# Performance work log

Hardware: AMD Instinct MI355X
Metric: run time of the kernel (lower is better)

The kernel has to match this reference:

```python
import jax, jax.numpy as jnp
import numpy as np

D_MODEL = 1024
N_HEADS = 16
D_FF = 4096
B, T = 4, 2048
EPS = 1e-5


def layernorm(x, g, b):
    mu = jnp.mean(x, axis=-1, keepdims=True)
    var = jnp.var(x, axis=-1, keepdims=True)
    return (x - mu) * jax.lax.rsqrt(var + EPS) * g + b


def setup_inputs() -> dict:
    key = jax.random.key(0)
    ks = jax.random.split(key, 8)
    s = 0.02
    return {
        "x": jax.random.normal(ks[0], (B, T, D_MODEL), jnp.float32),
        "ln1_g": jnp.ones((D_MODEL,), jnp.float32),
        "ln1_b": jnp.zeros((D_MODEL,), jnp.float32),
        "wq": jax.random.normal(ks[1], (D_MODEL, D_MODEL), jnp.float32) * s,
        "bq": jnp.zeros((D_MODEL,), jnp.float32),
        "wk": jax.random.normal(ks[2], (D_MODEL, D_MODEL), jnp.float32) * s,
        "bk": jnp.zeros((D_MODEL,), jnp.float32),
        "wv": jax.random.normal(ks[3], (D_MODEL, D_MODEL), jnp.float32) * s,
        "bv": jnp.zeros((D_MODEL,), jnp.float32),
        "wo": jax.random.normal(ks[4], (D_MODEL, D_MODEL), jnp.float32) * s,
        "bo": jnp.zeros((D_MODEL,), jnp.float32),
        "ln2_g": jnp.ones((D_MODEL,), jnp.float32),
        "ln2_b": jnp.zeros((D_MODEL,), jnp.float32),
        "w1": jax.random.normal(ks[5], (D_FF, D_MODEL), jnp.float32) * s,
        "b1": jnp.zeros((D_FF,), jnp.float32),
        "w2": jax.random.normal(ks[6], (D_MODEL, D_FF), jnp.float32) * s,
        "b2": jnp.zeros((D_MODEL,), jnp.float32),
    }


def reference(x, ln1_g, ln1_b, wq, bq, wk, bk, wv, bv, wo, bo,
              ln2_g, ln2_b, w1, b1, w2, b2):
    d_k = D_MODEL // N_HEADS
    # --- attention sublayer (pre-LN) ---
    h = layernorm(x, ln1_g, ln1_b)                       # [B,T,D]
    q = (h @ wq.T + bq).reshape(B, T, N_HEADS, d_k)
    k = (h @ wk.T + bk).reshape(B, T, N_HEADS, d_k)
    v = (h @ wv.T + bv).reshape(B, T, N_HEADS, d_k)
    scores = jnp.einsum("bqhd,bkhd->bhqk", q, k) / jnp.sqrt(jnp.float32(d_k))
    attn = jax.nn.softmax(scores, axis=-1)               # [B,H,T,T]
    o = jnp.einsum("bhqk,bkhd->bqhd", attn, v).reshape(B, T, D_MODEL)
    x = x + (o @ wo.T + bo)
    # --- FFN sublayer ---
    h2 = layernorm(x, ln2_g, ln2_b)
    h2 = jax.nn.gelu(h2 @ w1.T + b1, approximate=False)  # torch GELU = exact erf
    x = x + (h2 @ w2.T + b2)
    return x
```

## Files before the change

kernel.cpp:

```cpp
#include <hip/hip_runtime.h>
#include <math.h>


#define D_MODEL 1024
#define D_FF    4096
#define NH      16
#define BATCH   4
#define SEQ     2048
#define DK      64
#define MTOK    (BATCH*SEQ)
#define NBH     (BATCH*NH)

typedef __bf16 bf16;
typedef _Float16 f16;
typedef bf16  bf16x4 __attribute__((ext_vector_type(4)));
typedef bf16  bf16x8 __attribute__((ext_vector_type(8)));
typedef f16   f16x4  __attribute__((ext_vector_type(4)));
typedef f16   f16x8  __attribute__((ext_vector_type(8)));
typedef __fp16 hf16x2 __attribute__((ext_vector_type(2)));
typedef __fp16 hf16x4 __attribute__((ext_vector_type(4)));
typedef __fp16 hf16x8 __attribute__((ext_vector_type(8)));
typedef float f32x4  __attribute__((ext_vector_type(4)));

__device__ __forceinline__ void gload_lds16(const void* g, void* l) {
  __builtin_amdgcn_global_load_lds(
      (__attribute__((address_space(1))) void*)g,
      (__attribute__((address_space(3))) void*)l, 16, 0, 0);
}

#define BAR() __builtin_amdgcn_s_barrier()
#define LGKM0() do { asm volatile("s_waitcnt lgkmcnt(0)" ::: "memory"); \
  __builtin_amdgcn_sched_barrier(0); } while (0)
#define WAIT_VM0() do { asm volatile("s_waitcnt vmcnt(0)" ::: "memory"); \
  __builtin_amdgcn_sched_barrier(0); } while (0)
#define WAIT_VM4() do { asm volatile("s_waitcnt vmcnt(4)" ::: "memory"); \
  __builtin_amdgcn_sched_barrier(0); } while (0)

__device__ __forceinline__ float gelu_fast(float x) {
  float ax = fabsf(x) * 0.70710678118654752f;
  float t  = 1.0f / (1.0f + 0.3275911f * ax);
  float p  = t * (0.254829592f + t * (-0.284496736f + t * (1.421413741f +
             t * (-1.453152027f + t * 1.061405429f))));
  float e  = __builtin_amdgcn_exp2f(ax * ax * -1.4426950408889634f);
  float er = 1.0f - p * e;
  er = __builtin_copysignf(er, x);
  return 0.5f * x * (1.0f + er);
}

__global__ __launch_bounds__(256) void cast_w(const float* __restrict__ s,
                                              bf16* __restrict__ d, int n) {
  int i = (blockIdx.x * 256 + threadIdx.x) * 4;
  if (i >= n) return;
  float4 v = *(const float4*)(s + i);
  bf16x4 o;
  o[0] = (bf16)v.x; o[1] = (bf16)v.y; o[2] = (bf16)v.z; o[3] = (bf16)v.w;
  *(bf16x4*)(d + i) = o;
}

__global__ __launch_bounds__(256) void ln_kernel(const float* __restrict__ x,
                                                 const float* __restrict__ g,
                                                 const float* __restrict__ b,
                                                 bf16* __restrict__ out) {
  int row = blockIdx.x;
  int tid = threadIdx.x;
  const float* xr = x + (size_t)row * D_MODEL;
  float4 v = *(const float4*)(xr + tid * 4);
  float s  = v.x + v.y + v.z + v.w;
  float sq = v.x*v.x + v.y*v.y + v.z*v.z + v.w*v.w;
  #pragma unroll
  for (int off = 1; off < 64; off <<= 1) {
    s  += __shfl_xor(s,  off, 64);
    sq += __shfl_xor(sq, off, 64);
  }
  __shared__ float ls[4], lq[4];
  int wid = tid >> 6, lane = tid & 63;
  if (lane == 0) { ls[wid] = s; lq[wid] = sq; }
  __syncthreads();
  s  = ls[0] + ls[1] + ls[2] + ls[3];
  sq = lq[0] + lq[1] + lq[2] + lq[3];
  float mu   = s * (1.0f / D_MODEL);
  float var  = sq * (1.0f / D_MODEL) - mu * mu;
  float rstd = rsqrtf(var + 1e-5f);
  float4 gv = *(const float4*)(g + tid * 4);
  float4 bv = *(const float4*)(b + tid * 4);
  bf16x4 o;
  o[0] = (bf16)((v.x - mu) * rstd * gv.x + bv.x);
  o[1] = (bf16)((v.y - mu) * rstd * gv.y + bv.y);
  o[2] = (bf16)((v.z - mu) * rstd * gv.z + bv.z);
  o[3] = (bf16)((v.w - mu) * rstd * gv.w + bv.w);
  *(bf16x4*)(out + (size_t)row * D_MODEL + tid * 4) = o;
}

enum { EP_QKV = 0, EP_RESID = 1, EP_GELU = 2 };
#define QSCALE 0.18033688011112042f

template <int EP>
__global__ __launch_bounds__(512, 2) void gemm256(
    const bf16* __restrict__ A, const bf16* __restrict__ W,
    const float* __restrict__ bias,
    bf16* __restrict__ out_bf,
    int M, int N, int K) {
  __shared__ char lds[131072];
  int tiles_n = N >> 8;
  int nwg = (M >> 8) * tiles_n;
  int bid = blockIdx.x;
  int swz = (bid & 7) * (nwg >> 3) + (bid >> 3);
  int bm = swz / tiles_n, bn = swz % tiles_n;
  int m0 = bm << 8, n0 = bn << 8;
  int tid = threadIdx.x, wid = tid >> 6, lane = tid & 63;
  int wm = wid >> 2, wn = wid & 3;
  int l15 = lane & 15, l4 = lane >> 4;

  f32x4 acc[8][4];
  #pragma unroll
  for (int f = 0; f < 8; f++)
    #pragma unroll
    for (int n = 0; n < 4; n++)
      #pragma unroll
      for (int e = 0; e < 4; e++) acc[f][n][e] = 0.f;

  auto STAGEH = [&](int h, int kt, int bsel) {
    char* buf = lds + bsel * 65536;
    #pragma unroll
    for (int l = 0; l < 2; ++l) {
      int o = h * 16384 + l * 8192 + tid * 16;
      int row = (o >> 7) & 255;
      int g = (o >> 4) & 7;
      int gs = g ^ (row & 7);
      const bf16* src = (h < 2 ? A + (size_t)(m0 + row) * K
                               : W + (size_t)(n0 + row) * K) + kt * 64 + gs * 8;
      gload_lds16(src, buf + o);
    }
  };
  auto RDB = [&](const char* bc, int n, int kk) -> bf16x8 {
    int row = wn * 64 + n * 16 + l15;
    return *(const bf16x8*)(bc + 32768 + row * 128 + (((kk << 2) + l4) ^ (row & 7)) * 16);
  };

  int nt = K >> 6;
  STAGEH(0, 0, 0); STAGEH(1, 0, 0); STAGEH(2, 0, 0); STAGEH(3, 0, 0);
  STAGEH(0, 1, 1); STAGEH(1, 1, 1);
  WAIT_VM4();
  BAR();

  for (int t = 0; t < nt; ++t) {
    const char* bc = lds + (t & 1) * 65536;
    bf16x8 af[8][2];

    #pragma unroll
    for (int f = 0; f < 8; ++f)
      #pragma unroll
      for (int kk = 0; kk < 2; ++kk) {
        int row = wm * 128 + f * 16 + l15;
        af[f][kk] = *(const bf16x8*)(bc + row * 128 + (((kk << 2) + l4) ^ (row & 7)) * 16);
      }
    bf16x8 b0[2];
    b0[0] = RDB(bc, 0, 0); b0[1] = RDB(bc, 0, 1);
    if (t + 1 < nt) STAGEH(2, t + 1, (t + 1) & 1);
    BAR(); LGKM0();
    __builtin_amdgcn_s_setprio(1);
    #pragma unroll
    for (int f = 0; f < 8; ++f)
      #pragma unroll
      for (int kk = 0; kk < 2; ++kk) {
        if (EP == EP_QKV)
          acc[f][0] = __builtin_amdgcn_mfma_f32_16x16x32_bf16(af[f][kk], b0[kk], acc[f][0], 0, 0, 0);
        else
          acc[f][0] = __builtin_amdgcn_mfma_f32_16x16x32_bf16(b0[kk], af[f][kk], acc[f][0], 0, 0, 0);
      }
    __builtin_amdgcn_s_setprio(0);
    BAR();

    bf16x8 b1[2];
    b1[0] = RDB(bc, 1, 0); b1[1] = RDB(bc, 1, 1);
    if (t + 1 < nt) STAGEH(3, t + 1, (t + 1) & 1);
    BAR(); LGKM0();
    __builtin_amdgcn_s_setprio(1);
    #pragma unroll
    for (int f = 0; f < 8; ++f)
      #pragma unroll
      for (int kk = 0; kk < 2; ++kk) {
        if (EP == EP_QKV)
          acc[f][1] = __builtin_amdgcn_mfma_f32_16x16x32_bf16(af[f][kk], b1[kk], acc[f][1], 0, 0, 0);
        else
          acc[f][1] = __builtin_amdgcn_mfma_f32_16x16x32_bf16(b1[kk], af[f][kk], acc[f][1], 0, 0, 0);
      }
    __builtin_amdgcn_s_setprio(0);
    BAR();

    bf16x8 b2[2];
    b2[0] = RDB(bc, 2, 0); b2[1] = RDB(bc, 2, 1);
    if (t + 2 < nt) STAGEH(0, t + 2, t & 1);
    BAR(); LGKM0();
    __builtin_amdgcn_s_setprio(1);
    #pragma unroll
    for (int f = 0; f < 8; ++f)
      #pragma unroll
      for (int kk = 0; kk < 2; ++kk) {
        if (EP == EP_QKV)
          acc[f][2] = __builtin_amdgcn_mfma_f32_16x16x32_bf16(af[f][kk], b2[kk], acc[f][2], 0, 0, 0);
        else
          acc[f][2] = __builtin_amdgcn_mfma_f32_16x16x32_bf16(b2[kk], af[f][kk], acc[f][2], 0, 0, 0);
      }
    __builtin_amdgcn_s_setprio(0);
    BAR();

    bf16x8 b3[2];
    b3[0] = RDB(bc, 3, 0); b3[1] = RDB(bc, 3, 1);
    if (t + 2 < nt) STAGEH(1, t + 2, t & 1);
    BAR(); LGKM0();
    __builtin_amdgcn_s_setprio(1);
    #pragma unroll
    for (int f = 0; f < 8; ++f)
      #pragma unroll
      for (int kk = 0; kk < 2; ++kk) {
        if (EP == EP_QKV)
          acc[f][3] = __builtin_amdgcn_mfma_f32_16x16x32_bf16(af[f][kk], b3[kk], acc[f][3], 0, 0, 0);
        else
          acc[f][3] = __builtin_amdgcn_mfma_f32_16x16x32_bf16(b3[kk], af[f][kk], acc[f][3], 0, 0, 0);
      }
    __builtin_amdgcn_s_setprio(0);
    if (t + 2 < nt)      { WAIT_VM4(); }
    else if (t + 1 < nt) { WAIT_VM0(); }
    BAR();
  }

  if (EP == EP_QKV) {
    #pragma unroll
    for (int i = 0; i < 8; i++)
      #pragma unroll
      for (int j = 0; j < 4; j++) {
        int gm0 = m0 + wm * 128 + i * 16 + (l4 << 2);
        int gn  = n0 + wn * 64 + j * 16 + l15;
        int which = gn >> 10;
        int nn = gn & 1023, head = nn >> 6, d = nn & 63;
        int bb = gm0 >> 11, t = gm0 & 2047;
        float bv = bias[gn];
        if (which == 2) {
          int sbase = (t & ~31) + ((t >> 2) & 3) * 8 + ((t >> 4) & 1) * 4;
          f16x4 pk;
          #pragma unroll
          for (int jj = 0; jj < 4; jj++) pk[jj] = (f16)(acc[i][j][jj] + bv);
          *(f16x4*)((f16*)out_bf + (size_t)2 * NBH * SEQ * DK +
                    ((size_t)(bb * NH + head) * DK + d) * SEQ + sbase) = pk;
        } else {
          float scale = (which == 0) ? QSCALE : 1.0f;
          #pragma unroll
          for (int jj = 0; jj < 4; jj++) {
            float cv = (acc[i][j][jj] + bv) * scale;
            size_t idx = (size_t)which * (NBH * SEQ * DK) +
                         ((size_t)(bb * NH + head) * SEQ + (t + jj)) * DK + d;
            out_bf[idx] = (bf16)cv;
          }
        }
      }
  } else {
    #pragma unroll
    for (int i = 0; i < 8; i++) {
      int gm = m0 + wm * 128 + i * 16 + l15;
      #pragma unroll
      for (int j = 0; j < 4; j++) {
        int gn = n0 + wn * 64 + j * 16 + (l4 << 2);
        float4 bv4 = *(const float4*)(bias + gn);
        bf16x4 pk;
        pk[0] = (bf16)gelu_fast(acc[i][j][0] + bv4.x);
        pk[1] = (bf16)gelu_fast(acc[i][j][1] + bv4.y);
        pk[2] = (bf16)gelu_fast(acc[i][j][2] + bv4.z);
        pk[3] = (bf16)gelu_fast(acc[i][j][3] + bv4.w);
        *(bf16x4*)(out_bf + (size_t)gm * N + gn) = pk;
      }
    }
  }
}

__global__ __launch_bounds__(512) void gemm_resid(
    const bf16* __restrict__ A, const bf16* __restrict__ W,
    const float* __restrict__ bias,
    const float* __restrict__ resid,
    float* __restrict__ out_f32,
    int M, int N, int K) {
  constexpr int BK = 64, RB = 128;
  constexpr int AB = 16384, TB = 49152, L = 6;
  __shared__ char lds[3 * TB];

  int tiles_n = N >> 8;
  int nwg = (M >> 7) * tiles_n;
  int bid = blockIdx.x;
  int swz = (bid & 7) * (nwg >> 3) + (bid >> 3);
  int bm = swz / tiles_n, bn = swz % tiles_n;
  int m0 = bm << 7, n0 = bn << 8;
  int tid = threadIdx.x, wid = tid >> 6, lane = tid & 63;
  int wm = wid >> 2, wn = wid & 3;
  int l15 = lane & 15, l4 = lane >> 4;

  f32x4 acc[4][4];
  #pragma unroll
  for (int i = 0; i < 4; i++)
    #pragma unroll
    for (int j = 0; j < 4; j++)
      #pragma unroll
      for (int e = 0; e < 4; e++) acc[i][j][e] = 0.f;

  auto STAGE = [&](int kt, int nb) {
    char* buf = lds + nb * TB;
    #pragma unroll
    for (int l = 0; l < L; ++l) {
      bool isA = l < 2;
      int o = (isA ? l : l - 2) * 8192 + tid * 16;
      int row = o >> 7;
      int g = (o >> 4) & 7;
      int gs = g ^ (row & 7);
      const bf16* src = (isA ? A + (size_t)(m0 + row) * K
                             : W + (size_t)(n0 + row) * K) + kt * BK + gs * 8;
      gload_lds16(src, buf + (isA ? 0 : AB) + o);
    }
  };

  int nt = K / BK;
  STAGE(0, 0);
  STAGE(1, 1);
  asm volatile("s_waitcnt vmcnt(6)" ::: "memory");
  __builtin_amdgcn_sched_barrier(0);
  BAR();

  for (int t = 0; t < nt; ++t) {
    int cb = t % 3, nb = cb >= 1 ? cb - 1 : 2;
    const char* bc = lds + cb * TB;
    if (t + 2 < nt) STAGE(t + 2, nb);

    bf16x8 af[4][2], bfr[4][2];
    #pragma unroll
    for (int f = 0; f < 4; ++f)
      #pragma unroll
      for (int kk = 0; kk < 2; ++kk) {
        int row = wm * 64 + f * 16 + l15;
        af[f][kk] = *(const bf16x8*)(bc + row * RB + (((kk << 2) + l4) ^ (row & 7)) * 16);
      }
    #pragma unroll
    for (int fc = 0; fc < 4; ++fc)
      #pragma unroll
      for (int kk = 0; kk < 2; ++kk) {
        int row = wn * 64 + fc * 16 + l15;
        bfr[fc][kk] = *(const bf16x8*)(bc + AB + row * RB + (((kk << 2) + l4) ^ (row & 7)) * 16);
      }

    __builtin_amdgcn_s_setprio(1);
    #pragma unroll
    for (int f = 0; f < 4; ++f)
      #pragma unroll
      for (int fc = 0; fc < 4; ++fc)
        #pragma unroll
        for (int kk = 0; kk < 2; ++kk)
          acc[f][fc] = __builtin_amdgcn_mfma_f32_16x16x32_bf16(bfr[fc][kk], af[f][kk],
                                                               acc[f][fc], 0, 0, 0);
    __builtin_amdgcn_s_setprio(0);

    if (t + 2 < nt) {
      asm volatile("s_waitcnt vmcnt(6)" ::: "memory");
      __builtin_amdgcn_sched_barrier(0);
    } else if (t + 1 < nt) {
      WAIT_VM0();
    }
    BAR();
  }

  #pragma unroll
  for (int i = 0; i < 4; i++) {
    int gm = m0 + wm * 64 + i * 16 + l15;
    #pragma unroll
    for (int j = 0; j < 4; j++) {
      int gn = n0 + wn * 64 + j * 16 + (l4 << 2);
      float4 bv4 = *(const float4*)(bias + gn);
      size_t idx = (size_t)gm * N + gn;
      float4 rv = *(const float4*)(resid + idx);
      float4 ov;
      ov.x = rv.x + acc[i][j][0] + bv4.x;
      ov.y = rv.y + acc[i][j][1] + bv4.y;
      ov.z = rv.z + acc[i][j][2] + bv4.z;
      ov.w = rv.w + acc[i][j][3] + bv4.w;
      *(float4*)(out_f32 + idx) = ov;
    }
  }
}

__global__ __launch_bounds__(512) void attn_kernel(
    const bf16* __restrict__ q, const bf16* __restrict__ k,
    const f16* __restrict__ vt, bf16* __restrict__ o) {
  __shared__ bf16 kt_lds[2][64 * 64];
  __shared__ f16  vt_lds[2][64 * 64];
  int bid = blockIdx.x;
  int swzb = (bid & 7) * 64 + (bid >> 3);
  int bh = swzb >> 3;
  int qt = swzb & 7;
  int t0 = qt << 8;
  int tid = threadIdx.x, wid = tid >> 6, lane = tid & 63;
  int l15 = lane & 15, l4 = lane >> 4;

  int kb0 = l15 * 128 + ((l4 ^ (l15 & 7)) << 4);
  int kb1 = l15 * 128 + (((4 + l4) ^ (l15 & 7)) << 4);
  int vb32[2];
  #pragma unroll
  for (int n = 0; n < 2; n++)
    vb32[n] = l15 * 128 + (((n * 4 + l4) ^ (l15 & 7)) << 4);

  bf16x8 qf[2][2];
  #pragma unroll
  for (int qr = 0; qr < 2; qr++) {
    const bf16* qbase = q + ((size_t)bh * SEQ + t0 + wid * 32 + qr * 16 + l15) * DK;
    qf[qr][0] = *(const bf16x8*)(qbase + (l4 << 3));
    qf[qr][1] = *(const bf16x8*)(qbase + 32 + (l4 << 3));
  }

  f16x8 vones8;
  #pragma unroll
  for (int e = 0; e < 8; e++) vones8[e] = (f16)1.f;
  float m_run[2] = {-1e30f, -1e30f};
  f32x4 acc_o[2][4];
  f32x4 acc_l[2];
  #pragma unroll
  for (int qr = 0; qr < 2; qr++) {
    #pragma unroll
    for (int nd = 0; nd < 4; nd++)
      #pragma unroll
      for (int e = 0; e < 4; e++) acc_o[qr][nd][e] = 0.f;
    #pragma unroll
    for (int e = 0; e < 4; e++) acc_l[qr][e] = 0.f;
  }

  int oK = tid * 16;
  int rowk = oK >> 7, gk = (oK >> 4) & 7;
  const bf16* gKsrc = k + ((size_t)bh * SEQ + rowk) * DK + ((gk ^ (rowk & 7)) << 3);
  int dV = oK >> 7, gd = (oK >> 4) & 7;
  const f16* gVsrc = vt + ((size_t)bh * DK + dV) * SEQ + ((gd ^ (dV & 7)) << 3);

  auto stage = [&](int buf, int t) {
    int kv0 = t * 64;
    gload_lds16(gKsrc + (size_t)kv0 * DK, (char*)&kt_lds[buf][0] + tid * 16);
    gload_lds16(gVsrc + kv0, (char*)&vt_lds[buf][0] + tid * 16);
  };

  stage(0, 0);
  WAIT_VM0();
  BAR();

  for (int t = 0; t < SEQ / 64; ++t) {
    int cur = t & 1;
    if (t < SEQ / 64 - 1) stage(cur ^ 1, t + 1);
    const char* kbase = (const char*)&kt_lds[cur][0];
    const char* vbase = (const char*)&vt_lds[cur][0];

    f32x4 accs[2][4];
    #pragma unroll
    for (int qr = 0; qr < 2; qr++)
      #pragma unroll
      for (int n = 0; n < 4; n++)
        #pragma unroll
        for (int e = 0; e < 4; e++) accs[qr][n][e] = 0.f;
    __builtin_amdgcn_s_setprio(1);
    #pragma unroll
    for (int n = 0; n < 4; n++) {
      bf16x8 kf0 = *(const bf16x8*)(kbase + kb0 + n * 2048);
      bf16x8 kf1 = *(const bf16x8*)(kbase + kb1 + n * 2048);
      #pragma unroll
      for (int qr = 0; qr < 2; qr++) {
        accs[qr][n] = __builtin_amdgcn_mfma_f32_16x16x32_bf16(kf0, qf[qr][0], accs[qr][n], 0, 0, 0);
        accs[qr][n] = __builtin_amdgcn_mfma_f32_16x16x32_bf16(kf1, qf[qr][1], accs[qr][n], 0, 0, 0);
      }
    }
    __builtin_amdgcn_s_setprio(0);

    f16x8 pa32[2][2];
    #pragma unroll
    for (int qr = 0; qr < 2; qr++) {
      float mloc = -1e30f;
      #pragma unroll
      for (int n = 0; n < 4; n++) {
        float a0 = fmaxf(accs[qr][n][0], accs[qr][n][1]);
        float a1 = fmaxf(accs[qr][n][2], accs[qr][n][3]);
        mloc = fmaxf(mloc, fmaxf(a0, a1));
      }
      float mt = fmaxf(mloc, __shfl_xor(mloc, 16, 64));
      mt = fmaxf(mt, __shfl_xor(mt, 32, 64));
      if (__any(mt > m_run[qr] + 8.0f)) {
        float mn = fmaxf(m_run[qr], mt);
        float sc = __builtin_amdgcn_exp2f(m_run[qr] - mn);
        m_run[qr] = mn;
        float scr0 = __shfl(sc, l4 * 20 + 0, 64);
        float scr1 = __shfl(sc, l4 * 20 + 1, 64);
        float scr2 = __shfl(sc, l4 * 20 + 2, 64);
        float scr3 = __shfl(sc, l4 * 20 + 3, 64);
        #pragma unroll
        for (int nd = 0; nd < 4; nd++) {
          acc_o[qr][nd][0] *= scr0; acc_o[qr][nd][1] *= scr1;
          acc_o[qr][nd][2] *= scr2; acc_o[qr][nd][3] *= scr3;
        }
        acc_l[qr][0] *= scr0; acc_l[qr][1] *= scr1;
        acc_l[qr][2] *= scr2; acc_l[qr][3] *= scr3;
      }
      #pragma unroll
      for (int n = 0; n < 2; n++) {
        float e0 = __builtin_amdgcn_exp2f(accs[qr][2*n][0] - m_run[qr]);
        float e1 = __builtin_amdgcn_exp2f(accs[qr][2*n][1] - m_run[qr]);
        float e2 = __builtin_amdgcn_exp2f(accs[qr][2*n][2] - m_run[qr]);
        float e3 = __builtin_amdgcn_exp2f(accs[qr][2*n][3] - m_run[qr]);
        float e4 = __builtin_amdgcn_exp2f(accs[qr][2*n+1][0] - m_run[qr]);
        float e5 = __builtin_amdgcn_exp2f(accs[qr][2*n+1][1] - m_run[qr]);
        float e6 = __builtin_amdgcn_exp2f(accs[qr][2*n+1][2] - m_run[qr]);
        float e7 = __builtin_amdgcn_exp2f(accs[qr][2*n+1][3] - m_run[qr]);
        hf16x2 p01 = __builtin_amdgcn_cvt_pkrtz(e0, e1);
        hf16x2 p23 = __builtin_amdgcn_cvt_pkrtz(e2, e3);
        hf16x2 p45 = __builtin_amdgcn_cvt_pkrtz(e4, e5);
        hf16x2 p67 = __builtin_amdgcn_cvt_pkrtz(e6, e7);
        hf16x4 lo = __builtin_shufflevector(p01, p23, 0, 1, 2, 3);
        hf16x4 hi = __builtin_shufflevector(p45, p67, 0, 1, 2, 3);
        hf16x8 cmb = __builtin_shufflevector(lo, hi, 0, 1, 2, 3, 4, 5, 6, 7);
        pa32[qr][n] = __builtin_bit_cast(f16x8, cmb);
      }
    }

    __builtin_amdgcn_s_setprio(1);
    #pragma unroll
    for (int n = 0; n < 2; n++) {
      #pragma unroll
      for (int nd = 0; nd < 4; nd++) {
        f16x8 vf = *(const f16x8*)(vbase + vb32[n] + nd * 2048);
        #pragma unroll
        for (int qr = 0; qr < 2; qr++)
          acc_o[qr][nd] = __builtin_amdgcn_mfma_f32_16x16x32_f16(pa32[qr][n], vf, acc_o[qr][nd], 0, 0, 0);
      }
      #pragma unroll
      for (int qr = 0; qr < 2; qr++)
        acc_l[qr] = __builtin_amdgcn_mfma_f32_16x16x32_f16(pa32[qr][n], vones8, acc_l[qr], 0, 0, 0);
    }
    __builtin_amdgcn_s_setprio(0);

    if (t < SEQ / 64 - 1) { WAIT_VM0(); }
    BAR();
  }

  int bb = bh >> 4, hh = bh & 15;
  #pragma unroll
  for (int qr = 0; qr < 2; qr++) {
    float rl0 = 1.0f / acc_l[qr][0], rl1 = 1.0f / acc_l[qr][1];
    float rl2 = 1.0f / acc_l[qr][2], rl3 = 1.0f / acc_l[qr][3];
    int rowb = t0 + wid * 32 + qr * 16 + l4 * 4;
    #pragma unroll
    for (int nd = 0; nd < 4; nd++) {
      int d = nd * 16 + l15;
      o[((size_t)bb * SEQ + rowb + 0) * D_MODEL + hh * DK + d] = (bf16)(acc_o[qr][nd][0] * rl0);
      o[((size_t)bb * SEQ + rowb + 1) * D_MODEL + hh * DK + d] = (bf16)(acc_o[qr][nd][1] * rl1);
      o[((size_t)bb * SEQ + rowb + 2) * D_MODEL + hh * DK + d] = (bf16)(acc_o[qr][nd][2] * rl2);
      o[((size_t)bb * SEQ + rowb + 3) * D_MODEL + hh * DK + d] = (bf16)(acc_o[qr][nd][3] * rl3);
    }
  }
}

extern "C" void kernel_launch(void* const* d_in, const int* in_sizes, int n_in,
                              void* d_out, int out_size, void* d_ws, size_t ws_size,
                              hipStream_t stream) {
  const float* x    = (const float*)d_in[0];
  const float* ln1g = (const float*)d_in[1];
  const float* ln1b = (const float*)d_in[2];
  const float* wq   = (const float*)d_in[3];
  const float* bq   = (const float*)d_in[4];
  const float* wk   = (const float*)d_in[5];
  const float* bk   = (const float*)d_in[6];
  const float* wv   = (const float*)d_in[7];
  const float* bv   = (const float*)d_in[8];
  const float* wo   = (const float*)d_in[9];
  const float* bo   = (const float*)d_in[10];
  const float* ln2g = (const float*)d_in[11];
  const float* ln2b = (const float*)d_in[12];
  const float* w1   = (const float*)d_in[13];
  const float* b1   = (const float*)d_in[14];
  const float* w2   = (const float*)d_in[15];
  const float* b2   = (const float*)d_in[16];
  float* out = (float*)d_out;

  char* ws = (char*)d_ws;
  bf16* wqkv_b = (bf16*)(ws);
  bf16* wo_b   = (bf16*)(ws + ((size_t)6  << 20));
  bf16* w1_b   = (bf16*)(ws + ((size_t)8  << 20));
  bf16* w2_b   = (bf16*)(ws + ((size_t)16 << 20));
  bf16* h_b    = (bf16*)(ws + ((size_t)24 << 20));
  bf16* qkv_b  = (bf16*)(ws + ((size_t)40 << 20));
  bf16* o_b    = (bf16*)(ws + ((size_t)88 << 20));
  bf16* ffn1_b = (bf16*)(ws + ((size_t)40 << 20));
  float* bqkv  = (float*)(ws + ((size_t)104 << 20));

  cast_w<<<1024, 256, 0, stream>>>(wq, wqkv_b, 1 << 20);
  cast_w<<<1024, 256, 0, stream>>>(wk, wqkv_b + (1 << 20), 1 << 20);
  cast_w<<<1024, 256, 0, stream>>>(wv, wqkv_b + (2 << 20), 1 << 20);
  cast_w<<<1024, 256, 0, stream>>>(wo, wo_b, 1 << 20);
  cast_w<<<4096, 256, 0, stream>>>(w1, w1_b, 1 << 22);
  cast_w<<<4096, 256, 0, stream>>>(w2, w2_b, 1 << 22);
  (void)hipMemcpyAsync(bqkv,        bq, 4096, hipMemcpyDeviceToDevice, stream);
  (void)hipMemcpyAsync(bqkv + 1024, bk, 4096, hipMemcpyDeviceToDevice, stream);
  (void)hipMemcpyAsync(bqkv + 2048, bv, 4096, hipMemcpyDeviceToDevice, stream);

  ln_kernel<<<MTOK, 256, 0, stream>>>(x, ln1g, ln1b, h_b);
  gemm256<EP_QKV><<<384, 512, 0, stream>>>(h_b, wqkv_b, bqkv, qkv_b,
                                           MTOK, 3072, 1024);
  attn_kernel<<<512, 512, 0, stream>>>(qkv_b, qkv_b + (size_t)NBH * SEQ * DK,
                                       (const f16*)(qkv_b + (size_t)2 * NBH * SEQ * DK),
                                       o_b);
  gemm_resid<<<256, 512, 0, stream>>>(o_b, wo_b, bo, x, out, MTOK, 1024, 1024);
  ln_kernel<<<MTOK, 256, 0, stream>>>(out, ln2g, ln2b, h_b);
  gemm256<EP_GELU><<<512, 512, 0, stream>>>(h_b, w1_b, b1, ffn1_b,
                                            MTOK, 4096, 1024);
  gemm_resid<<<256, 512, 0, stream>>>(ffn1_b, w2_b, b2, out, out, MTOK, 1024, 4096);
}
```

Baseline: 392.8 us.

## Fuse weight casts and bias copies into one launch; reorder GEMM fragment loads

Replaces six weight-cast kernel launches and three device-to-device bias memcpys with a single fused kernel, cutting launch and copy overhead. Separately, the gemm256 main loop now loads the A fragments in two halves of four, interleaved with pairs of B fragments across the four phases. This lowers peak register use, at the cost of rereading some B fragments from LDS.

```diff
diff --git a/kernel.cpp b/kernel.cpp
--- a/kernel.cpp
+++ b/kernel.cpp
@@ -47,14 +47,41 @@
   return 0.5f * x * (1.0f + er);
 }
 
-__global__ __launch_bounds__(256) void cast_w(const float* __restrict__ s,
-                                              bf16* __restrict__ d, int n) {
-  int i = (blockIdx.x * 256 + threadIdx.x) * 4;
-  if (i >= n) return;
-  float4 v = *(const float4*)(s + i);
+__global__ __launch_bounds__(256) void fused_cast(
+    const float* __restrict__ wq, const float* __restrict__ wk,
+    const float* __restrict__ wv, const float* __restrict__ wo,
+    const float* __restrict__ w1, const float* __restrict__ w2,
+    const float* __restrict__ bq, const float* __restrict__ bk,
+    const float* __restrict__ bv,
+    bf16* __restrict__ wqkv_b, bf16* __restrict__ wo_b,
+    bf16* __restrict__ w1_b, bf16* __restrict__ w2_b,
+    float* __restrict__ bqkv) {
+  int b = blockIdx.x;
+  if (b >= 12288) {
+    int which = b - 12288;
+    const float* s = (which == 0) ? bq : (which == 1) ? bk : bv;
+    int i = threadIdx.x * 4;
+    *(float4*)(bqkv + which * 1024 + i) = *(const float4*)(s + i);
+    return;
+  }
+  size_t i = ((size_t)b * 256 + threadIdx.x) * 4;
+  int seg = (int)(i >> 20);
+  const float* src;
+  bf16* dst;
+  if (seg < 3) {
+    src = (seg == 0 ? wq : seg == 1 ? wk : wv) + (i & 0xFFFFF);
+    dst = wqkv_b + i;
+  } else if (seg == 3) {
+    src = wo + (i - (3u << 20));  dst = wo_b + (i - (3u << 20));
+  } else if (seg < 8) {
+    src = w1 + (i - (4u << 20));  dst = w1_b + (i - (4u << 20));
+  } else {
+    src = w2 + (i - (8u << 20));  dst = w2_b + (i - (8u << 20));
+  }
+  float4 v = *(const float4*)src;
   bf16x4 o;
   o[0] = (bf16)v.x; o[1] = (bf16)v.y; o[2] = (bf16)v.z; o[3] = (bf16)v.w;
-  *(bf16x4*)(d + i) = o;
+  *(bf16x4*)dst = o;
 }
 
 __global__ __launch_bounds__(256) void ln_kernel(const float* __restrict__ x,
@@ -132,9 +159,17 @@
       gload_lds16(src, buf + o);
     }
   };
+  auto RDA = [&](const char* bc, int f, int kk) -> bf16x8 {
+    int row = wm * 128 + f * 16 + l15;
+    return *(const bf16x8*)(bc + row * 128 + (((kk << 2) + l4) ^ (row & 7)) * 16);
+  };
   auto RDB = [&](const char* bc, int n, int kk) -> bf16x8 {
     int row = wn * 64 + n * 16 + l15;
     return *(const bf16x8*)(bc + 32768 + row * 128 + (((kk << 2) + l4) ^ (row & 7)) * 16);
+  };
+  auto MM = [&](f32x4& a, bf16x8 av, bf16x8 bv) {
+    if (EP == EP_QKV) a = __builtin_amdgcn_mfma_f32_16x16x32_bf16(av, bv, a, 0, 0, 0);
+    else              a = __builtin_amdgcn_mfma_f32_16x16x32_bf16(bv, av, a, 0, 0, 0);
   };
 
   int nt = K >> 6;
@@ -143,82 +178,65 @@
   WAIT_VM4();
   BAR();
 
+  bf16x8 af[4][2], bq[2][2];
   for (int t = 0; t < nt; ++t) {
     const char* bc = lds + (t & 1) * 65536;
-    bf16x8 af[8][2];
-
-    #pragma unroll
-    for (int f = 0; f < 8; ++f)
-      #pragma unroll
-      for (int kk = 0; kk < 2; ++kk) {
-        int row = wm * 128 + f * 16 + l15;
-        af[f][kk] = *(const bf16x8*)(bc + row * 128 + (((kk << 2) + l4) ^ (row & 7)) * 16);
-      }
-    bf16x8 b0[2];
-    b0[0] = RDB(bc, 0, 0); b0[1] = RDB(bc, 0, 1);
+
+    #pragma unroll
+    for (int f = 0; f < 4; ++f) { af[f][0] = RDA(bc, f, 0); af[f][1] = RDA(bc, f, 1); }
+    #pragma unroll
+    for (int j = 0; j < 2; ++j) { bq[j][0] = RDB(bc, j, 0); bq[j][1] = RDB(bc, j, 1); }
     if (t + 1 < nt) STAGEH(2, t + 1, (t + 1) & 1);
     BAR(); LGKM0();
     __builtin_amdgcn_s_setprio(1);
     #pragma unroll
-    for (int f = 0; f < 8; ++f)
-      #pragma unroll
-      for (int kk = 0; kk < 2; ++kk) {
-        if (EP == EP_QKV)
-          acc[f][0] = __builtin_amdgcn_mfma_f32_16x16x32_bf16(af[f][kk], b0[kk], acc[f][0], 0, 0, 0);
-        else
-          acc[f][0] = __builtin_amdgcn_mfma_f32_16x16x32_bf16(b0[kk], af[f][kk], acc[f][0], 0, 0, 0);
-      }
+    for (int f = 0; f < 4; ++f)
+      #pragma unroll
+      for (int j = 0; j < 2; ++j)
+        #pragma unroll
+        for (int kk = 0; kk < 2; ++kk) MM(acc[f][j], af[f][kk], bq[j][kk]);
     __builtin_amdgcn_s_setprio(0);
     BAR();
 
-    bf16x8 b1[2];
-    b1[0] = RDB(bc, 1, 0); b1[1] = RDB(bc, 1, 1);
+    #pragma unroll
+    for (int j = 0; j < 2; ++j) { bq[j][0] = RDB(bc, 2 + j, 0); bq[j][1] = RDB(bc, 2 + j, 1); }
     if (t + 1 < nt) STAGEH(3, t + 1, (t + 1) & 1);
     BAR(); LGKM0();
     __builtin_amdgcn_s_setprio(1);
     #pragma unroll
-    for (int f = 0; f < 8; ++f)
-      #pragma unroll
-      for (int kk = 0; kk < 2; ++kk) {
-        if (EP == EP_QKV)
-          acc[f][1] = __builtin_amdgcn_mfma_f32_16x16x32_bf16(af[f][kk], b1[kk], acc[f][1], 0, 0, 0);
-        else
-          acc[f][1] = __builtin_amdgcn_mfma_f32_16x16x32_bf16(b1[kk], af[f][kk], acc[f][1], 0, 0, 0);
-      }
+    for (int f = 0; f < 4; ++f)
+      #pragma unroll
+      for (int j = 0; j < 2; ++j)
+        #pragma unroll
+        for (int kk = 0; kk < 2; ++kk) MM(acc[f][2 + j], af[f][kk], bq[j][kk]);
     __builtin_amdgcn_s_setprio(0);
     BAR();
 
-    bf16x8 b2[2];
-    b2[0] = RDB(bc, 2, 0); b2[1] = RDB(bc, 2, 1);
+    #pragma unroll
+    for (int f = 0; f < 4; ++f) { af[f][0] = RDA(bc, 4 + f, 0); af[f][1] = RDA(bc, 4 + f, 1); }
     if (t + 2 < nt) STAGEH(0, t + 2, t & 1);
     BAR(); LGKM0();
     __builtin_amdgcn_s_setprio(1);
     #pragma unroll
-    for (int f = 0; f < 8; ++f)
-      #pragma unroll
-      for (int kk = 0; kk < 2; ++kk) {
-        if (EP == EP_QKV)
-          acc[f][2] = __builtin_amdgcn_mfma_f32_16x16x32_bf16(af[f][kk], b2[kk], acc[f][2], 0, 0, 0);
-        else
-          acc[f][2] = __builtin_amdgcn_mfma_f32_16x16x32_bf16(b2[kk], af[f][kk], acc[f][2], 0, 0, 0);
-      }
+    for (int f = 0; f < 4; ++f)
+      #pragma unroll
+      for (int j = 0; j < 2; ++j)
+        #pragma unroll
+        for (int kk = 0; kk < 2; ++kk) MM(acc[4 + f][2 + j], af[f][kk], bq[j][kk]);
     __builtin_amdgcn_s_setprio(0);
     BAR();
 
-    bf16x8 b3[2];
-    b3[0] = RDB(bc, 3, 0); b3[1] = RDB(bc, 3, 1);
+    #pragma unroll
+    for (int j = 0; j < 2; ++j) { bq[j][0] = RDB(bc, j, 0); bq[j][1] = RDB(bc, j, 1); }
     if (t + 2 < nt) STAGEH(1, t + 2, t & 1);
     BAR(); LGKM0();
     __builtin_amdgcn_s_setprio(1);
     #pragma unroll
-    for (int f = 0; f < 8; ++f)
-      #pragma unroll
-      for (int kk = 0; kk < 2; ++kk) {
-        if (EP == EP_QKV)
-          acc[f][3] = __builtin_amdgcn_mfma_f32_16x16x32_bf16(af[f][kk], b3[kk], acc[f][3], 0, 0, 0);
-        else
-          acc[f][3] = __builtin_amdgcn_mfma_f32_16x16x32_bf16(b3[kk], af[f][kk], acc[f][3], 0, 0, 0);
-      }
+    for (int f = 0; f < 4; ++f)
+      #pragma unroll
+      for (int j = 0; j < 2; ++j)
+        #pragma unroll
+        for (int kk = 0; kk < 2; ++kk) MM(acc[4 + f][j], af[f][kk], bq[j][kk]);
     __builtin_amdgcn_s_setprio(0);
     if (t + 2 < nt)      { WAIT_VM4(); }
     else if (t + 1 < nt) { WAIT_VM0(); }
@@ -588,16 +606,8 @@
   bf16* ffn1_b = (bf16*)(ws + ((size_t)40 << 20));
   float* bqkv  = (float*)(ws + ((size_t)104 << 20));
 
-  cast_w<<<1024, 256, 0, stream>>>(wq, wqkv_b, 1 << 20);
-  cast_w<<<1024, 256, 0, stream>>>(wk, wqkv_b + (1 << 20), 1 << 20);
-  cast_w<<<1024, 256, 0, stream>>>(wv, wqkv_b + (2 << 20), 1 << 20);
-  cast_w<<<1024, 256, 0, stream>>>(wo, wo_b, 1 << 20);
-  cast_w<<<4096, 256, 0, stream>>>(w1, w1_b, 1 << 22);
-  cast_w<<<4096, 256, 0, stream>>>(w2, w2_b, 1 << 22);
-  (void)hipMemcpyAsync(bqkv,        bq, 4096, hipMemcpyDeviceToDevice, stream);
-  (void)hipMemcpyAsync(bqkv + 1024, bk, 4096, hipMemcpyDeviceToDevice, stream);
-  (void)hipMemcpyAsync(bqkv + 2048, bv, 4096, hipMemcpyDeviceToDevice, stream);
-
+  fused_cast<<<12291, 256, 0, stream>>>(wq, wk, wv, wo, w1, w2, bq, bk, bv,
+                                        wqkv_b, wo_b, w1_b, w2_b, bqkv);
   ln_kernel<<<MTOK, 256, 0, stream>>>(x, ln1g, ln1b, h_b);
   gemm256<EP_QKV><<<384, 512, 0, stream>>>(h_b, wqkv_b, bqkv, qkv_b,
                                            MTOK, 3072, 1024);
```

After: 382.1 us. -2.7%, faster.
